# Optimization experiments

Hardware: AMD Instinct MI355X
Metric: run time of the kernel (lower is better)

## Reference

```python
import jax, jax.numpy as jnp
import numpy as np

EMBED_DIM = 1024
NUM_HEADS = 16
HEAD_DIM = EMBED_DIM // NUM_HEADS
SCALING = HEAD_DIM ** -0.5


def setup_inputs() -> dict:
    key = jax.random.key(0)
    ks = jax.random.split(key, 10)
    B, T, D = 4, 2048, EMBED_DIM
    s = 0.02
    return {
        "hidden_states": jax.random.normal(ks[0], (B, T, D), jnp.float32),
        "attention_mask": jnp.zeros((B, 1, T, T), jnp.float32),
        "Wq": jax.random.normal(ks[1], (D, D), jnp.float32) * s,
        "bq": jnp.zeros((D,), jnp.float32),
        "Wk": jax.random.normal(ks[2], (D, D), jnp.float32) * s,
        "bk": jnp.zeros((D,), jnp.float32),
        "Wv": jax.random.normal(ks[3], (D, D), jnp.float32) * s,
        "bv": jnp.zeros((D,), jnp.float32),
        "Wo": jax.random.normal(ks[4], (D, D), jnp.float32) * s,
        "bo": jnp.zeros((D,), jnp.float32),
    }


def reference(hidden_states, attention_mask, Wq, bq, Wk, bk, Wv, bv, Wo, bo):
    B, T, D = hidden_states.shape
    H, Hd = NUM_HEADS, HEAD_DIM
    # projections (torch Linear: x @ W.T + b; here W stored as (D_in, D_out))
    q = (hidden_states @ Wq + bq) * SCALING
    k = hidden_states @ Wk + bk
    v = hidden_states @ Wv + bv
    q = q.reshape(B, T, H, Hd).transpose(0, 2, 1, 3)  # [B,H,T,Hd]
    k = k.reshape(B, T, H, Hd).transpose(0, 2, 1, 3)
    v = v.reshape(B, T, H, Hd).transpose(0, 2, 1, 3)
    # eager attention: full [B,H,T,T] scores + additive mask + softmax
    scores = jnp.einsum("bhtd,bhsd->bhts", q, k)
    scores = scores + attention_mask[:, :, :, : k.shape[2]]
    attn_weights = jax.nn.softmax(scores, axis=-1)
    attn_output = jnp.einsum("bhts,bhsd->bhtd", attn_weights, v)
    attn_output = attn_output.transpose(0, 2, 1, 3).reshape(B, T, D)
    attn_output = attn_output @ Wo + bo
    return attn_output
```

## Files before the change

kernel.cpp:

```cpp
#include <hip/hip_runtime.h>
#include <hip/hip_bf16.h>
#include <cstdint>

#define TT 2048
#define DD 1024
#define NH 16
#define HD 64
#define NB 4
#define SCALING 0.125f
#define LOG2E 1.44269504088896340736f
#define QSCALE (0.125f * 1.44269504088896340736f)

typedef __bf16 bf16;
typedef __attribute__((ext_vector_type(8))) __bf16 bf16x8;
typedef __attribute__((ext_vector_type(4))) __bf16 bf16x4;
typedef __attribute__((ext_vector_type(4))) float f32x4;

__device__ __forceinline__ void gload_lds16(const bf16* g, bf16* l) {
    __builtin_amdgcn_global_load_lds(
        (__attribute__((address_space(1))) const void*)g,
        (__attribute__((address_space(3))) void*)l, 16, 0, 0);
}

__global__ __launch_bounds__(256) void k_prep(const float* __restrict__ x, bf16* __restrict__ xb,
                                              const float* __restrict__ Wq, const float* __restrict__ Wk,
                                              const float* __restrict__ Wv, const float* __restrict__ Wo,
                                              bf16* __restrict__ Wt) {
    __shared__ float tile_s[32][33];
    int bid = blockIdx.x, tid = threadIdx.x;
    if (bid < 8192) {
        size_t i = ((size_t)bid * 256 + tid) * 4;
        float4 v = *(const float4*)(x + i);
        bf16x4 o;
        o[0] = (bf16)v.x; o[1] = (bf16)v.y; o[2] = (bf16)v.z; o[3] = (bf16)v.w;
        *(bf16x4*)(xb + i) = o;
        return;
    }
    int b2 = bid - 8192;
    int mat = b2 >> 10, tl = b2 & 1023;
    int n0 = (tl & 31) * 32, k0 = (tl >> 5) * 32;
    const float* w = mat == 0 ? Wq : (mat == 1 ? Wk : (mat == 2 ? Wv : Wo));
    int tx = tid & 31, ty = tid >> 5;
#pragma unroll
    for (int i = 0; i < 4; i++)
        tile_s[ty + 8 * i][tx] = w[(size_t)(k0 + ty + 8 * i) * DD + n0 + tx];
    __syncthreads();
#pragma unroll
    for (int i = 0; i < 4; i++)
        Wt[(size_t)mat * DD * DD + (size_t)(n0 + ty + 8 * i) * DD + k0 + tx] = (bf16)tile_s[tx][ty + 8 * i];
}

__device__ __forceinline__ void gemm128_main(const bf16* __restrict__ A, const bf16* __restrict__ Bt,
                                             int m0, int n0, int K,
                                             bf16* As, bf16* Bs, f32x4 acc[4][4]) {
    const int tid = threadIdx.x;
    const int w = tid >> 6, lane = tid & 63;
    const int wr = w >> 1, wc = w & 1, quad = lane >> 4, l16 = lane & 15;
    f32x4 zero = {0.f, 0.f, 0.f, 0.f};
#pragma unroll
    for (int mi = 0; mi < 4; mi++)
#pragma unroll
        for (int ni = 0; ni < 4; ni++) acc[mi][ni] = zero;

    for (int k0 = 0; k0 < K; k0 += 32) {
        if (k0) __syncthreads();
#pragma unroll
        for (int j = 0; j < 2; j++) {
            int idx = w * 128 + j * 64 + lane;
            int row = idx >> 2, kc = (idx & 3) * 8;
            gload_lds16(A + (size_t)(m0 + row) * K + k0 + kc, As + idx * 8);
            gload_lds16(Bt + (size_t)(n0 + row) * K + k0 + kc, Bs + idx * 8);
        }
        __syncthreads();
        bf16x8 af[4], bfv[4];
#pragma unroll
        for (int i = 0; i < 4; i++)
            af[i] = *(const bf16x8*)(As + (wr * 64 + i * 16 + l16) * 32 + quad * 8);
#pragma unroll
        for (int i = 0; i < 4; i++)
            bfv[i] = *(const bf16x8*)(Bs + (wc * 64 + i * 16 + l16) * 32 + quad * 8);
#pragma unroll
        for (int mi = 0; mi < 4; mi++)
#pragma unroll
            for (int ni = 0; ni < 4; ni++)
                acc[mi][ni] = __builtin_amdgcn_mfma_f32_16x16x32_bf16(af[mi], bfv[ni], acc[mi][ni], 0, 0, 0);
    }
}

__global__ __launch_bounds__(256) void k_gemm_qkv(const bf16* __restrict__ Xb, const bf16* __restrict__ Wt,
                                                  const float* __restrict__ bq, const float* __restrict__ bk,
                                                  const float* __restrict__ bv,
                                                  bf16* __restrict__ qb, bf16* __restrict__ kb,
                                                  bf16* __restrict__ vt,
                                                  const float* __restrict__ mask, int* __restrict__ flags) {
    __shared__ bf16 smem[8448];
    __shared__ int s_any[4];
    const int bid = blockIdx.x, tid = threadIdx.x;
    const int grp = bid / 7, rem = bid % 7;

    if (rem >= 3) {
        int fid = grp * 4 + (rem - 3);
        int st = fid & 31, tt = (fid >> 5) & 15, bbm = fid >> 9;
        const float* mp = mask + ((size_t)bbm * TT + tt * 128) * TT + st * 64;
        int c = (tid & 15) * 4;
        int r0 = tid >> 4;
        int any = 0;
        for (int r = r0; r < 128; r += 16) {
            float4 v = *(const float4*)(mp + (size_t)r * TT + c);
            any |= (v.x != 0.f) | (v.y != 0.f) | (v.z != 0.f) | (v.w != 0.f);
        }
        any = __any(any) ? 1 : 0;
        if ((tid & 63) == 0) s_any[tid >> 6] = any;
        __syncthreads();
        if (tid == 0)
            flags[(bbm * 16 + tt) * 32 + st] = s_any[0] | s_any[1] | s_any[2] | s_any[3];
        return;
    }

    int g = grp * 3 + rem;
    int bx = g % 24, by = g / 24;
    int m0 = by * 128, n0 = bx * 128;
    bf16* As = smem;
    bf16* Bs = smem + 4096;
    f32x4 acc[4][4];
    gemm128_main(Xb, Wt, m0, n0, DD, As, Bs, acc);

    const int w = tid >> 6, lane = tid & 63;
    const int wr = w >> 1, wc = w & 1, quad = lane >> 4, l16 = lane & 15;
    const int which = n0 >> 10;
    const int bbk = m0 >> 11, tbase = m0 & 2047;

    if (which < 2) {
        const float* bias = which == 0 ? bq : bk;
#pragma unroll
        for (int mi = 0; mi < 4; mi++)
#pragma unroll
            for (int ni = 0; ni < 4; ni++) {
                int nn = (n0 & 1023) + wc * 64 + ni * 16 + l16;
                int h = nn >> 6, d = nn & 63;
                float bb_ = bias[nn];
#pragma unroll
                for (int r = 0; r < 4; r++) {
                    int t = tbase + wr * 64 + mi * 16 + quad * 4 + r;
                    float v = acc[mi][ni][r] + bb_;
                    if (which == 0)
                        qb[(((size_t)bbk * NH + h) * TT + t) * HD + d] = (bf16)(v * QSCALE);
                    else
                        kb[(((size_t)bbk * NH + h) * TT + t) * HD + d] = (bf16)v;
                }
            }
    } else {
        const int nn0 = n0 & 1023;
#pragma unroll
        for (int phase = 0; phase < 2; phase++) {
            __syncthreads();
            if (wc == phase) {
#pragma unroll
                for (int mi = 0; mi < 4; mi++)
#pragma unroll
                    for (int ni = 0; ni < 4; ni++) {
                        int nn_l = ni * 16 + l16;
                        float bb_ = bv[nn0 + phase * 64 + nn_l];
#pragma unroll
                        for (int r = 0; r < 4; r++) {
                            int t_l = wr * 64 + mi * 16 + quad * 4 + r;
                            smem[nn_l * 132 + t_l] = (bf16)(acc[mi][ni][r] + bb_);
                        }
                    }
            }
            __syncthreads();
            int hh = (nn0 + phase * 64) >> 6;
#pragma unroll
            for (int i = 0; i < 4; i++) {
                int idx = i * 256 + tid;
                int rr = idx >> 4, cc = (idx & 15) * 8;
                bf16x8 vv = *(const bf16x8*)(smem + rr * 132 + cc);
                *(bf16x8*)(vt + (((size_t)bbk * NH + hh) * HD + rr) * TT + tbase + cc) = vv;
            }
        }
    }
}

__global__ __launch_bounds__(256) void k_attn(const bf16* __restrict__ qb, const bf16* __restrict__ kb,
                                              const bf16* __restrict__ vt, const float* __restrict__ mask,
                                              const int* __restrict__ flags, bf16* __restrict__ ob) {
    __shared__ bf16 Qs[128 * 64];
    __shared__ bf16 Ks[64 * 64];
    __shared__ bf16 Vs[64 * 64];

    const int tq0 = blockIdx.x * 128;
    const int h = blockIdx.y, bb = blockIdx.z;
    const int tid = threadIdx.x, w = tid >> 6, lane = tid & 63;
    const int quad = lane >> 4, l16 = lane & 15;

    const bf16* Qg = qb + (((size_t)bb * NH + h) * TT + tq0) * HD;
    const bf16* Kg = kb + ((size_t)bb * NH + h) * TT * HD;
    const bf16* Vg = vt + ((size_t)bb * NH + h) * HD * TT;

#pragma unroll
    for (int j = 0; j < 4; j++) {
        int idx = (w * 4 + j) * 64 + lane;
        int row = idx >> 3, cs = idx & 7;
        gload_lds16(Qg + (size_t)row * HD + (cs ^ (row & 7)) * 8, Qs + idx * 8);
    }

    bf16x8 ones;
#pragma unroll
    for (int i = 0; i < 8; i++) ones[i] = (bf16)1.0f;

    f32x4 oa[2][4];
    f32x4 lacc[2];
    f32x4 zero = {0.f, 0.f, 0.f, 0.f};
#pragma unroll
    for (int qi = 0; qi < 2; qi++) {
        lacc[qi] = zero;
#pragma unroll
        for (int ni = 0; ni < 4; ni++) oa[qi][ni] = zero;
    }

    const int fbase = (bb * 16 + blockIdx.x) * 32;
    const int vkey = l16 & 14;

    for (int s0 = 0; s0 < TT; s0 += 64) {
        __syncthreads();
#pragma unroll
        for (int j = 0; j < 2; j++) {
            int idx = (w * 2 + j) * 64 + lane;
            int row = idx >> 3, m = idx & 7;
            gload_lds16(Kg + (size_t)(s0 + row) * HD + (m ^ (row & 7)) * 8, Ks + idx * 8);
            gload_lds16(Vg + (size_t)row * TT + s0 + ((2 * m) ^ (row & 14)) * 4, Vs + idx * 8);
        }
        __syncthreads();

        f32x4 st[4][2];
#pragma unroll
        for (int si = 0; si < 4; si++)
#pragma unroll
            for (int qi = 0; qi < 2; qi++) st[si][qi] = zero;
#pragma unroll
        for (int kd = 0; kd < 2; kd++) {
            const int csw = ((kd * 4 + quad) ^ (l16 & 7)) * 8;
            bf16x8 kf[4], qf[2];
#pragma unroll
            for (int si = 0; si < 4; si++)
                kf[si] = *(const bf16x8*)(Ks + (si * 16 + l16) * 64 + csw);
#pragma unroll
            for (int qi = 0; qi < 2; qi++)
                qf[qi] = *(const bf16x8*)(Qs + (w * 32 + qi * 16 + l16) * 64 + csw);
#pragma unroll
            for (int si = 0; si < 4; si++)
#pragma unroll
                for (int qi = 0; qi < 2; qi++)
                    st[si][qi] = __builtin_amdgcn_mfma_f32_16x16x32_bf16(kf[si], qf[qi], st[si][qi], 0, 0, 0);
        }

        if (flags[fbase + (s0 >> 6)]) {
            const float* mp = mask + ((size_t)bb * TT + tq0) * TT + s0;
#pragma unroll
            for (int si = 0; si < 4; si++)
#pragma unroll
                for (int qi = 0; qi < 2; qi++)
#pragma unroll
                    for (int r = 0; r < 4; r++)
                        st[si][qi][r] += mp[(size_t)(w * 32 + qi * 16 + l16) * TT + si * 16 + quad * 4 + r] * LOG2E;
        }

        bf16 ep[4][2][4];
#pragma unroll
        for (int si = 0; si < 4; si++)
#pragma unroll
            for (int qi = 0; qi < 2; qi++)
#pragma unroll
                for (int r = 0; r < 4; r++)
                    ep[si][qi][r] = (bf16)exp2f(st[si][qi][r]);

#pragma unroll
        for (int kk = 0; kk < 2; kk++) {
            bf16x8 ap[2];
#pragma unroll
            for (int qi = 0; qi < 2; qi++)
#pragma unroll
                for (int j = 0; j < 8; j++)
                    ap[qi][j] = ep[2 * kk + (j >> 2)][qi][j & 3];
            bf16x8 bv8[4];
#pragma unroll
            for (int ni = 0; ni < 4; ni++) {
                const int rbase = (ni * 16 + l16) * 64;
                const int c0 = ((kk * 8 + quad) ^ vkey) * 4;
                const int c1 = ((kk * 8 + quad + 4) ^ vkey) * 4;
                bf16x4 lo = *(const bf16x4*)(Vs + rbase + c0);
                bf16x4 hi = *(const bf16x4*)(Vs + rbase + c1);
#pragma unroll
                for (int e = 0; e < 4; e++) { bv8[ni][e] = lo[e]; bv8[ni][e + 4] = hi[e]; }
            }
#pragma unroll
            for (int qi = 0; qi < 2; qi++)
                lacc[qi] = __builtin_amdgcn_mfma_f32_16x16x32_bf16(ap[qi], ones, lacc[qi], 0, 0, 0);
#pragma unroll
            for (int qi = 0; qi < 2; qi++)
#pragma unroll
                for (int ni = 0; ni < 4; ni++)
                    oa[qi][ni] = __builtin_amdgcn_mfma_f32_16x16x32_bf16(ap[qi], bv8[ni], oa[qi][ni], 0, 0, 0);
        }
    }

#pragma unroll
    for (int qi = 0; qi < 2; qi++)
#pragma unroll
        for (int r = 0; r < 4; r++) {
            float inv = 1.f / lacc[qi][r];
            int trow = tq0 + w * 32 + qi * 16 + quad * 4 + r;
#pragma unroll
            for (int ni = 0; ni < 4; ni++) {
                float v = oa[qi][ni][r] * inv;
                ob[((size_t)bb * TT + trow) * DD + h * HD + ni * 16 + l16] = (bf16)v;
            }
        }
}

__global__ __launch_bounds__(256) void k_gemm_out(const bf16* __restrict__ Ob, const bf16* __restrict__ Wot,
                                                  const float* __restrict__ bo, float* __restrict__ out) {
    __shared__ bf16 As[128 * 32];
    __shared__ bf16 Bs[128 * 32];
    int m0 = blockIdx.y * 128, n0 = blockIdx.x * 128;
    f32x4 acc[4][4];
    gemm128_main(Ob, Wot, m0, n0, DD, As, Bs, acc);

    const int tid = threadIdx.x, w = tid >> 6, lane = tid & 63;
    const int wr = w >> 1, wc = w & 1, quad = lane >> 4, l16 = lane & 15;
#pragma unroll
    for (int mi = 0; mi < 4; mi++)
#pragma unroll
        for (int ni = 0; ni < 4; ni++) {
            int gn = n0 + wc * 64 + ni * 16 + l16;
            float bb_ = bo[gn];
#pragma unroll
            for (int r = 0; r < 4; r++) {
                int gm = m0 + wr * 64 + mi * 16 + quad * 4 + r;
                out[(size_t)gm * DD + gn] = acc[mi][ni][r] + bb_;
            }
        }
}

extern "C" void kernel_launch(void* const* d_in, const int* in_sizes, int n_in,
                              void* d_out, int out_size, void* d_ws, size_t ws_size,
                              hipStream_t stream) {
    const float* hidden = (const float*)d_in[0];
    const float* mask   = (const float*)d_in[1];
    const float* Wq     = (const float*)d_in[2];
    const float* bq     = (const float*)d_in[3];
    const float* Wk     = (const float*)d_in[4];
    const float* bk     = (const float*)d_in[5];
    const float* Wv     = (const float*)d_in[6];
    const float* bv     = (const float*)d_in[7];
    const float* Wo     = (const float*)d_in[8];
    const float* bo     = (const float*)d_in[9];
    float* out = (float*)d_out;
    char* ws = (char*)d_ws;

    const size_t MB = 1024 * 1024;
    bf16* Xb   = (bf16*)(ws);
    bf16* Wt   = (bf16*)(ws + 16 * MB);
    bf16* qb   = (bf16*)(ws + 24 * MB);
    bf16* kb   = (bf16*)(ws + 40 * MB);
    bf16* vt   = (bf16*)(ws + 56 * MB);
    bf16* ob   = (bf16*)(ws + 72 * MB);
    int* flags = (int*)(ws + 88 * MB);

    hipLaunchKernelGGL(k_prep, dim3(12288), dim3(256), 0, stream, hidden, Xb, Wq, Wk, Wv, Wo, Wt);
    hipLaunchKernelGGL(k_gemm_qkv, dim3(3584), dim3(256), 0, stream, Xb, Wt, bq, bk, bv, qb, kb, vt, mask, flags);
    hipLaunchKernelGGL(k_attn, dim3(16, 16, 4), dim3(256), 0, stream, qb, kb, vt, mask, flags, ob);
    hipLaunchKernelGGL(k_gemm_out, dim3(8, 64), dim3(256), 0, stream, ob, Wt + (size_t)3 * DD * DD, bo, out);
}
```

Before: 404.7 us.

## Double-buffer K/V tiles in attention and keep Q fragments in registers

Restructures the attention loop so the next K/V tile is loaded asynchronously into a second LDS buffer while the current tile is computed, removing one barrier per iteration. Q fragments are loaded into registers once, and the Q LDS region is reused as a buffer afterwards. The V^T tile layout changes so each lane reads one 16-byte chunk instead of two 8-byte reads, and the V projection store order is permuted to match. Mask flags are checked once per block so fully unmasked blocks skip the per-tile flag loads. The kernel also adds a launch_bounds occupancy hint of 4, which may cost registers.

```diff
diff --git a/kernel.cpp b/kernel.cpp
--- a/kernel.cpp
+++ b/kernel.cpp
@@ -162,10 +162,8 @@
                         int nn_l = ni * 16 + l16;
                         float bb_ = bv[nn0 + phase * 64 + nn_l];
 #pragma unroll
-                        for (int r = 0; r < 4; r++) {
-                            int t_l = wr * 64 + mi * 16 + quad * 4 + r;
-                            smem[nn_l * 132 + t_l] = (bf16)(acc[mi][ni][r] + bb_);
-                        }
+                        for (int r = 0; r < 4; r++)
+                            smem[nn_l * 132 + wr * 64 + quad * 16 + mi * 4 + r] = (bf16)(acc[mi][ni][r] + bb_);
                     }
             }
             __syncthreads();
@@ -181,12 +179,11 @@
     }
 }
 
-__global__ __launch_bounds__(256) void k_attn(const bf16* __restrict__ qb, const bf16* __restrict__ kb,
-                                              const bf16* __restrict__ vt, const float* __restrict__ mask,
-                                              const int* __restrict__ flags, bf16* __restrict__ ob) {
-    __shared__ bf16 Qs[128 * 64];
-    __shared__ bf16 Ks[64 * 64];
-    __shared__ bf16 Vs[64 * 64];
+__global__ __launch_bounds__(256, 4) void k_attn(const bf16* __restrict__ qb, const bf16* __restrict__ kb,
+                                                 const bf16* __restrict__ vt, const float* __restrict__ mask,
+                                                 const int* __restrict__ flags, bf16* __restrict__ ob) {
+    __shared__ bf16 SB[4][4096];
+    __shared__ int s_anyflag;
 
     const int tq0 = blockIdx.x * 128;
     const int h = blockIdx.y, bb = blockIdx.z;
@@ -197,11 +194,32 @@
     const bf16* Kg = kb + ((size_t)bb * NH + h) * TT * HD;
     const bf16* Vg = vt + ((size_t)bb * NH + h) * HD * TT;
 
+    int cidx[2], koff[2], voff[2];
+#pragma unroll
+    for (int j = 0; j < 2; j++) {
+        int idx = (w * 2 + j) * 64 + lane;
+        int row = idx >> 3, m = idx & 7;
+        cidx[j] = idx * 8;
+        koff[j] = row * HD + ((m ^ (row & 7)) * 8);
+        voff[j] = row * TT + ((m ^ (row & 7)) * 8);
+    }
+
 #pragma unroll
     for (int j = 0; j < 4; j++) {
         int idx = (w * 4 + j) * 64 + lane;
-        int row = idx >> 3, cs = idx & 7;
-        gload_lds16(Qg + (size_t)row * HD + (cs ^ (row & 7)) * 8, Qs + idx * 8);
+        int row = idx >> 3, m = idx & 7;
+        gload_lds16(Qg + row * HD + (m ^ (row & 7)) * 8, &SB[2][0] + idx * 8);
+    }
+#pragma unroll
+    for (int j = 0; j < 2; j++) {
+        gload_lds16(Kg + koff[j], SB[0] + cidx[j]);
+        gload_lds16(Vg + voff[j], SB[1] + cidx[j]);
+    }
+
+    const int fbase = (bb * 16 + blockIdx.x) * 32;
+    {
+        int f0 = (tid < 32) ? flags[fbase + tid] : 0;
+        if (tid < 64) { int a = __any(f0 != 0) ? 1 : 0; if (tid == 0) s_anyflag = a; }
     }
 
     bf16x8 ones;
@@ -218,91 +236,88 @@
         for (int ni = 0; ni < 4; ni++) oa[qi][ni] = zero;
     }
 
-    const int fbase = (bb * 16 + blockIdx.x) * 32;
-    const int vkey = l16 & 14;
-
-    for (int s0 = 0; s0 < TT; s0 += 64) {
+    __syncthreads();
+    const int anyflag = s_anyflag;
+
+    bf16x8 aq[2][2];
+#pragma unroll
+    for (int kd = 0; kd < 2; kd++) {
+        const int csw = ((kd * 4 + quad) ^ (l16 & 7)) * 8;
+#pragma unroll
+        for (int qi = 0; qi < 2; qi++)
+            aq[kd][qi] = *(const bf16x8*)(&SB[2][0] + (w * 32 + qi * 16 + l16) * 64 + csw);
+    }
+
+#define ATTN_COMPUTE(Ks, Vs, S0)                                                              \
+    {                                                                                         \
+        f32x4 st[4][2];                                                                       \
+        _Pragma("unroll") for (int si = 0; si < 4; si++)                                      \
+            _Pragma("unroll") for (int qi = 0; qi < 2; qi++) st[si][qi] = zero;               \
+        _Pragma("unroll") for (int kd = 0; kd < 2; kd++) {                                    \
+            const int csw = ((kd * 4 + quad) ^ (l16 & 7)) * 8;                                \
+            bf16x8 kf[4];                                                                     \
+            _Pragma("unroll") for (int si = 0; si < 4; si++)                                  \
+                kf[si] = *(const bf16x8*)((Ks) + (si * 16 + l16) * 64 + csw);                 \
+            _Pragma("unroll") for (int si = 0; si < 4; si++)                                  \
+                _Pragma("unroll") for (int qi = 0; qi < 2; qi++)                              \
+                    st[si][qi] = __builtin_amdgcn_mfma_f32_16x16x32_bf16(kf[si], aq[kd][qi],  \
+                                                                        st[si][qi], 0, 0, 0);\
+        }                                                                                     \
+        if (anyflag && flags[fbase + ((S0) >> 6)]) {                                          \
+            const float* mp = mask + ((size_t)bb * TT + tq0) * TT + (S0);                     \
+            _Pragma("unroll") for (int si = 0; si < 4; si++)                                  \
+                _Pragma("unroll") for (int qi = 0; qi < 2; qi++)                              \
+                    _Pragma("unroll") for (int r = 0; r < 4; r++)                             \
+                        st[si][qi][r] += mp[(size_t)(w * 32 + qi * 16 + l16) * TT             \
+                                            + si * 16 + quad * 4 + r] * LOG2E;                \
+        }                                                                                     \
+        bf16 ep[4][2][4];                                                                     \
+        _Pragma("unroll") for (int si = 0; si < 4; si++)                                      \
+            _Pragma("unroll") for (int qi = 0; qi < 2; qi++)                                  \
+                _Pragma("unroll") for (int r = 0; r < 4; r++)                                 \
+                    ep[si][qi][r] = (bf16)exp2f(st[si][qi][r]);                               \
+        _Pragma("unroll") for (int kk = 0; kk < 2; kk++) {                                    \
+            bf16x8 ap[2];                                                                     \
+            _Pragma("unroll") for (int qi = 0; qi < 2; qi++)                                  \
+                _Pragma("unroll") for (int j = 0; j < 8; j++)                                 \
+                    ap[qi][j] = ep[2 * kk + (j >> 2)][qi][j & 3];                             \
+            bf16x8 bv8[4];                                                                    \
+            _Pragma("unroll") for (int ni = 0; ni < 4; ni++)                                  \
+                bv8[ni] = *(const bf16x8*)((Vs) + (ni * 16 + l16) * 64                        \
+                                           + ((quad * 2 + kk) ^ (l16 & 7)) * 8);              \
+            _Pragma("unroll") for (int qi = 0; qi < 2; qi++)                                  \
+                lacc[qi] = __builtin_amdgcn_mfma_f32_16x16x32_bf16(ap[qi], ones, lacc[qi],    \
+                                                                   0, 0, 0);                  \
+            _Pragma("unroll") for (int qi = 0; qi < 2; qi++)                                  \
+                _Pragma("unroll") for (int ni = 0; ni < 4; ni++)                              \
+                    oa[qi][ni] = __builtin_amdgcn_mfma_f32_16x16x32_bf16(ap[qi], bv8[ni],     \
+                                                                         oa[qi][ni], 0, 0, 0);\
+        }                                                                                     \
+    }
+
+    ATTN_COMPUTE(SB[0], SB[1], 0)
+    __syncthreads();
+#pragma unroll
+    for (int j = 0; j < 2; j++) {
+        gload_lds16(Kg + 64 * HD + koff[j], SB[2] + cidx[j]);
+        gload_lds16(Vg + 64 + voff[j], SB[3] + cidx[j]);
+    }
+    __syncthreads();
+
+    for (int i = 1; i < 32; i++) {
+        const int cur = i & 1, nxt = cur ^ 1;
+        if (i < 31) {
+            const int sn = (i + 1) * 64;
+#pragma unroll
+            for (int j = 0; j < 2; j++) {
+                gload_lds16(Kg + sn * HD + koff[j], SB[2 * nxt] + cidx[j]);
+                gload_lds16(Vg + sn + voff[j], SB[2 * nxt + 1] + cidx[j]);
+            }
+        }
+        ATTN_COMPUTE(SB[2 * cur], SB[2 * cur + 1], i * 64)
         __syncthreads();
-#pragma unroll
-        for (int j = 0; j < 2; j++) {
-            int idx = (w * 2 + j) * 64 + lane;
-            int row = idx >> 3, m = idx & 7;
-            gload_lds16(Kg + (size_t)(s0 + row) * HD + (m ^ (row & 7)) * 8, Ks + idx * 8);
-            gload_lds16(Vg + (size_t)row * TT + s0 + ((2 * m) ^ (row & 14)) * 4, Vs + idx * 8);
-        }
-        __syncthreads();
-
-        f32x4 st[4][2];
-#pragma unroll
-        for (int si = 0; si < 4; si++)
-#pragma unroll
-            for (int qi = 0; qi < 2; qi++) st[si][qi] = zero;
-#pragma unroll
-        for (int kd = 0; kd < 2; kd++) {
-            const int csw = ((kd * 4 + quad) ^ (l16 & 7)) * 8;
-            bf16x8 kf[4], qf[2];
-#pragma unroll
-            for (int si = 0; si < 4; si++)
-                kf[si] = *(const bf16x8*)(Ks + (si * 16 + l16) * 64 + csw);
-#pragma unroll
-            for (int qi = 0; qi < 2; qi++)
-                qf[qi] = *(const bf16x8*)(Qs + (w * 32 + qi * 16 + l16) * 64 + csw);
-#pragma unroll
-            for (int si = 0; si < 4; si++)
-#pragma unroll
-                for (int qi = 0; qi < 2; qi++)
-                    st[si][qi] = __builtin_amdgcn_mfma_f32_16x16x32_bf16(kf[si], qf[qi], st[si][qi], 0, 0, 0);
-        }
-
-        if (flags[fbase + (s0 >> 6)]) {
-            const float* mp = mask + ((size_t)bb * TT + tq0) * TT + s0;
-#pragma unroll
-            for (int si = 0; si < 4; si++)
-#pragma unroll
-                for (int qi = 0; qi < 2; qi++)
-#pragma unroll
-                    for (int r = 0; r < 4; r++)
-                        st[si][qi][r] += mp[(size_t)(w * 32 + qi * 16 + l16) * TT + si * 16 + quad * 4 + r] * LOG2E;
-        }
-
-        bf16 ep[4][2][4];
-#pragma unroll
-        for (int si = 0; si < 4; si++)
-#pragma unroll
-            for (int qi = 0; qi < 2; qi++)
-#pragma unroll
-                for (int r = 0; r < 4; r++)
-                    ep[si][qi][r] = (bf16)exp2f(st[si][qi][r]);
-
-#pragma unroll
-        for (int kk = 0; kk < 2; kk++) {
-            bf16x8 ap[2];
-#pragma unroll
-            for (int qi = 0; qi < 2; qi++)
-#pragma unroll
-                for (int j = 0; j < 8; j++)
-                    ap[qi][j] = ep[2 * kk + (j >> 2)][qi][j & 3];
-            bf16x8 bv8[4];
-#pragma unroll
-            for (int ni = 0; ni < 4; ni++) {
-                const int rbase = (ni * 16 + l16) * 64;
-                const int c0 = ((kk * 8 + quad) ^ vkey) * 4;
-                const int c1 = ((kk * 8 + quad + 4) ^ vkey) * 4;
-                bf16x4 lo = *(const bf16x4*)(Vs + rbase + c0);
-                bf16x4 hi = *(const bf16x4*)(Vs + rbase + c1);
-#pragma unroll
-                for (int e = 0; e < 4; e++) { bv8[ni][e] = lo[e]; bv8[ni][e + 4] = hi[e]; }
-            }
-#pragma unroll
-            for (int qi = 0; qi < 2; qi++)
-                lacc[qi] = __builtin_amdgcn_mfma_f32_16x16x32_bf16(ap[qi], ones, lacc[qi], 0, 0, 0);
-#pragma unroll
-            for (int qi = 0; qi < 2; qi++)
-#pragma unroll
-                for (int ni = 0; ni < 4; ni++)
-                    oa[qi][ni] = __builtin_amdgcn_mfma_f32_16x16x32_bf16(ap[qi], bv8[ni], oa[qi][ni], 0, 0, 0);
-        }
-    }
+    }
+#undef ATTN_COMPUTE
 
 #pragma unroll
     for (int qi = 0; qi < 2; qi++)
```

New measurement: 376.6 us. 6.9% less time.
